# Kernel tuning notes

Hardware: AMD Instinct MI355X
Metric: run time of the kernel (lower is better)

The kernel has to match this reference:

```python
import jax, jax.numpy as jnp
import numpy as np
import math

NUM_BUCKETS = 32
MAX_DISTANCE = 128
N_HEADS = 16
D_KV = 64
ATTN_SCALE = True


def _relative_position_bucket(relative_position, num_buckets=NUM_BUCKETS, max_distance=MAX_DISTANCE):
    # bidirectional (encoder) variant
    nb = num_buckets // 2
    buckets = (relative_position > 0).astype(jnp.int32) * nb
    rp = jnp.abs(relative_position)
    max_exact = nb // 2
    is_small = rp < max_exact
    rp_large = max_exact + (
        jnp.log(rp.astype(jnp.float32) / max_exact)
        / math.log(max_distance / max_exact)
        * (nb - max_exact)
    ).astype(jnp.int32)
    rp_large = jnp.minimum(rp_large, nb - 1)
    buckets = buckets + jnp.where(is_small, rp, rp_large)
    return buckets


def compute_bias(rel_bias_emb, q_len, k_len):
    ctx = jnp.arange(q_len)[:, None]
    mem = jnp.arange(k_len)[None, :]
    bucket = _relative_position_bucket(mem - ctx)  # [q,k] int32 in [0,32)
    values = rel_bias_emb[bucket]                  # [q,k,H]
    return jnp.transpose(values, (2, 0, 1))[None]  # [1,H,q,k]


def setup_inputs() -> dict:
    key = jax.random.key(0)
    k1, k2, k3, k4 = jax.random.split(key, 4)
    B, S, D = 2, 2048, 1024
    return {
        "hidden_states": jax.random.normal(k1, (B, S, D), jnp.float32),
        "attention_mask": jnp.ones((B, 1, S, S), jnp.float32),
        "W_qkv": jax.random.normal(k2, (D, 3 * D), jnp.float32) * 0.02,
        "W_o": jax.random.normal(k3, (D, D), jnp.float32) * 0.02,
        "rel_bias_emb": jax.random.normal(k4, (NUM_BUCKETS, N_HEADS), jnp.float32) * 0.02,
    }


def reference(hidden_states, attention_mask, W_qkv, W_o, rel_bias_emb):
    B, S, D = hidden_states.shape
    # fused QKV projection (no bias), then split as in split_tensor_along_last_dim
    qkv = jnp.einsum("bsd,de->bse", hidden_states, W_qkv)
    q, k, v = jnp.split(qkv, 3, axis=-1)
    # [b,s,H*d] -> [b,H,s,d]
    def to_heads(t):
        return jnp.transpose(t.reshape(B, S, N_HEADS, D_KV), (0, 2, 1, 3))
    q, k, v = to_heads(q), to_heads(k), to_heads(v)
    scores = jnp.einsum("bhqd,bhkd->bhqk", q, k)
    if ATTN_SCALE:
        scores = scores / math.sqrt(D_KV)
    position_bias = compute_bias(rel_bias_emb, S, S)  # [1,H,S,S]
    scores = scores * attention_mask + (-10000.0 * (1.0 - attention_mask) + position_bias)
    probs = jax.nn.softmax(scores, axis=-1)  # dropout = eval mode (identity)
    ctx = jnp.einsum("bhqk,bhkd->bhqd", probs, v)
    ctx = jnp.transpose(ctx, (0, 2, 1, 3)).reshape(B, S, N_HEADS * D_KV)
    attn_output = jnp.einsum("bse,ed->bsd", ctx, W_o)
    return attn_output
```

## Files before the change

### kernel.cpp

```cpp
#include <hip/hip_runtime.h>
#include <cstdint>

#define DEV static __device__ __forceinline__

typedef __bf16 bf16x8 __attribute__((ext_vector_type(8)));
typedef __bf16 bf16x4 __attribute__((ext_vector_type(4)));
typedef short  s16x4  __attribute__((ext_vector_type(4)));
typedef float  f32x4  __attribute__((ext_vector_type(4)));

#define VM_WAIT4 asm volatile("s_waitcnt vmcnt(4)" ::: "memory")
#define VM_WAIT3 asm volatile("s_waitcnt vmcnt(3)" ::: "memory")
#define VM_WAIT0 asm volatile("s_waitcnt vmcnt(0)" ::: "memory")

DEV unsigned short f32_bf16(float f) {
  union { float f; unsigned u; } v; v.f = f;
  unsigned r = v.u + 0x7FFFu + ((v.u >> 16) & 1u);
  return (unsigned short)(r >> 16);
}

DEV void gload16(const void* g, void* lds) {
  __builtin_amdgcn_global_load_lds((__attribute__((address_space(1))) void*)g,
                                   (__attribute__((address_space(3))) void*)lds,
                                   16, 0, 0);
}

DEV float bcast_lane(float v, int srclane) {
  union { float f; int i; } u; u.f = v;
  u.i = __builtin_amdgcn_ds_bpermute(srclane << 2, u.i);
  return u.f;
}

DEV void transpose_body(const float* __restrict__ W, unsigned short* __restrict__ WT,
                        int K, int N, int k0, int n0, float (*t)[65]) {
  int tn = threadIdx.x & 63, tk = threadIdx.x >> 6;
#pragma unroll
  for (int i = 0; i < 64; i += 4)
    t[tk + i][tn] = W[(size_t)(k0 + tk + i) * N + n0 + tn];
  __syncthreads();
  int k2 = (threadIdx.x & 31) * 2, n = threadIdx.x >> 5;
#pragma unroll
  for (int i = 0; i < 64; i += 8) {
    int nn = n + i;
    unsigned o = (unsigned)f32_bf16(t[k2][nn]) | ((unsigned)f32_bf16(t[k2 + 1][nn]) << 16);
    *(unsigned*)&WT[(size_t)(n0 + nn) * K + k0 + k2] = o;
  }
}

__global__ void __launch_bounds__(256) prologue(const float* __restrict__ hs,
                                                unsigned short* __restrict__ hB,
                                                const float* __restrict__ wqkv,
                                                unsigned short* __restrict__ wqT,
                                                const float* __restrict__ wo,
                                                unsigned short* __restrict__ woT,
                                                const float* __restrict__ mask,
                                                int* __restrict__ flag) {
  __shared__ float t[64][65];
  const int bid = blockIdx.x;
  if (bid < 4096) {
    int i = bid * 256 + threadIdx.x;
    float4 v = ((const float4*)hs)[i];
    uint2 o;
    o.x = (unsigned)f32_bf16(v.x) | ((unsigned)f32_bf16(v.y) << 16);
    o.y = (unsigned)f32_bf16(v.z) | ((unsigned)f32_bf16(v.w) << 16);
    ((uint2*)hB)[i] = o;
  } else if (bid < 4864) {
    int tt = bid - 4096;
    transpose_body(wqkv, wqT, 1024, 3072, (tt & 15) * 64, (tt >> 4) * 64, t);
  } else if (bid < 5120) {
    int tt = bid - 4864;
    transpose_body(wo, woT, 1024, 1024, (tt & 15) * 64, (tt >> 4) * 64, t);
  } else {
    size_t i = ((size_t)(bid - 5120) * 256 + threadIdx.x) * 4;
    float4 v = *(const float4*)(mask + i);
    if (v.x != 1.0f || v.y != 1.0f || v.z != 1.0f || v.w != 1.0f) atomicOr(flag, 1);
  }
}

template <int MODE, int TN, bool TRANS>
DEV void gemm_body(const unsigned short* __restrict__ A,
                   const unsigned short* __restrict__ BT,
                   float* __restrict__ Cout,
                   unsigned short* __restrict__ Qb,
                   unsigned short* __restrict__ Kb,
                   unsigned short* __restrict__ VTb,
                   int bm, int bn, int M, int N, int K,
                   unsigned short* As, unsigned short* Bs) {
  constexpr int NT = TN / 32;
  constexpr int ASZ = 128 * 32, BSZ = TN * 32;
  const int tid = threadIdx.x, wave = tid >> 6, lane = tid & 63;
  const int l = lane & 15, quad = lane >> 4;
  const int wm = (wave & 1) * 64, wn = (wave >> 1) * (TN >> 1);

  const int srowA = wave * 32 + (lane >> 2);
  const int sswzA = ((lane & 3) ^ (srowA & 3)) * 8;
  const int srowB = (TN == 128) ? srowA : (wave * 16 + (lane >> 2));
  const int sswzB = ((lane & 3) ^ (srowB & 3)) * 8;
  const unsigned short* pA = A + (size_t)(bm * 128 + srowA) * K + sswzA;
  const unsigned short* pB = BT + (size_t)(bn * TN + srowB) * K + sswzB;
  const int ldsA0 = (wave * 32) * 32;
  const int ldsA1 = (wave * 32 + 16) * 32;
  const int ldsB0 = (TN == 128 ? wave * 32 : wave * 16) * 32;
  const int ldsB1 = (wave * 32 + 16) * 32;

  auto stage = [&](int buf) {
    gload16(pA, &As[buf * ASZ + ldsA0]);
    gload16(pA + (size_t)16 * K, &As[buf * ASZ + ldsA1]);
    gload16(pB, &Bs[buf * BSZ + ldsB0]);
    if (TN == 128) gload16(pB + (size_t)16 * K, &Bs[buf * BSZ + ldsB1]);
    pA += 32; pB += 32;
  };

  f32x4 acc[4][NT];
#pragma unroll
  for (int i = 0; i < 4; i++)
#pragma unroll
    for (int j = 0; j < NT; j++) { f32x4 z = {0.f, 0.f, 0.f, 0.f}; acc[i][j] = z; }

  stage(0);
  stage(1);

  const int nkt = K >> 5;
  for (int kt = 0; kt < nkt; kt++) {
    const int cur = kt % 3;
    if (kt != nkt - 1) {
      if (TN == 128) { VM_WAIT4; } else { VM_WAIT3; }
    } else {
      VM_WAIT0;
    }
    __builtin_amdgcn_s_barrier();
    __builtin_amdgcn_sched_barrier(0);
    if (kt + 2 < nkt) stage((kt + 2) % 3);
    bf16x8 af[4], bv[NT];
#pragma unroll
    for (int mt = 0; mt < 4; mt++) {
      int r = wm + mt * 16 + l;
      af[mt] = *(const bf16x8*)&As[cur * ASZ + r * 32 + ((quad ^ (r & 3)) * 8)];
    }
#pragma unroll
    for (int nt = 0; nt < NT; nt++) {
      int r = wn + nt * 16 + l;
      bv[nt] = *(const bf16x8*)&Bs[cur * BSZ + r * 32 + ((quad ^ (r & 3)) * 8)];
    }
#pragma unroll
    for (int mt = 0; mt < 4; mt++)
#pragma unroll
      for (int nt = 0; nt < NT; nt++) {
        if (TRANS)
          acc[mt][nt] = __builtin_amdgcn_mfma_f32_16x16x32_bf16(bv[nt], af[mt], acc[mt][nt], 0, 0, 0);
        else
          acc[mt][nt] = __builtin_amdgcn_mfma_f32_16x16x32_bf16(af[mt], bv[nt], acc[mt][nt], 0, 0, 0);
      }
  }

#pragma unroll
  for (int nt = 0; nt < NT; nt++) {
#pragma unroll
    for (int mt = 0; mt < 4; mt++) {
      if (TRANS) {
        const int s = bm * 128 + wm + mt * 16 + l;
        const int col = bn * TN + wn + nt * 16 + quad * 4;
        if (MODE == 0) {
          *(float4*)&Cout[(size_t)s * N + col] = *(float4*)&acc[mt][nt];
        } else {
          const int bb = s >> 11, sl = s & 2047;
          unsigned short* dst = (col < 1024) ? Qb : Kb;
          const int c = col & 1023;
          const size_t off = ((size_t)(bb * 16 + (c >> 6)) * 2048 + sl) * 64 + (c & 63);
          bf16x4 pk;
#pragma unroll
          for (int r = 0; r < 4; r++) pk[r] = (__bf16)acc[mt][nt][r];
          *(bf16x4*)&dst[off] = pk;
        }
      } else {
        const int col = bn * TN + wn + nt * 16 + l;
        const int row0 = bm * 128 + wm + mt * 16 + quad * 4;
        const int bb = row0 >> 11, s = row0 & 2047;
        const int c = col - 2048;
        const int sl = s & 127;
        const int snew = (s & ~127) | (sl & 0x63) | ((sl & 0x0C) << 1) | ((sl & 0x10) >> 2);
        const size_t off = ((size_t)(bb * 16 + (c >> 6)) * 64 + (c & 63)) * 2048 + snew;
        bf16x4 pk;
#pragma unroll
        for (int r = 0; r < 4; r++) pk[r] = (__bf16)acc[mt][nt][r];
        *(bf16x4*)&VTb[off] = pk;
      }
    }
  }
}

__global__ void __launch_bounds__(256) gemm_qkv(const unsigned short* __restrict__ A,
                                                const unsigned short* __restrict__ BT,
                                                unsigned short* __restrict__ Qb,
                                                unsigned short* __restrict__ Kb,
                                                unsigned short* __restrict__ VTb,
                                                int M, int N, int K) {
  __shared__ __align__(16) unsigned short As[3][128 * 32];
  __shared__ __align__(16) unsigned short Bs[3][128 * 32];
  const int bm = blockIdx.x, bn = blockIdx.y;
  if (bn < 16)
    gemm_body<2, 128, true>(A, BT, nullptr, Qb, Kb, VTb, bm, bn, M, N, K, &As[0][0], &Bs[0][0]);
  else
    gemm_body<2, 128, false>(A, BT, nullptr, Qb, Kb, VTb, bm, bn, M, N, K, &As[0][0], &Bs[0][0]);
}

__global__ void __launch_bounds__(256) gemm_out(const unsigned short* __restrict__ A,
                                                const unsigned short* __restrict__ BT,
                                                float* __restrict__ Cout,
                                                int M, int N, int K) {
  __shared__ __align__(16) unsigned short As[3][128 * 32];
  __shared__ __align__(16) unsigned short Bs[3][64 * 32];
  gemm_body<0, 64, true>(A, BT, Cout, nullptr, nullptr, nullptr,
                         blockIdx.x, blockIdx.y, M, N, K, &As[0][0], &Bs[0][0]);
}

__global__ void __launch_bounds__(512, 4) attn(const unsigned short* __restrict__ Qb,
                                               const unsigned short* __restrict__ Kb,
                                               const unsigned short* __restrict__ VTb,
                                               const float* __restrict__ mask,
                                               const float* __restrict__ emb,
                                               const int* __restrict__ mflag,
                                               unsigned short* __restrict__ ctx) {
  __shared__ __align__(16) unsigned short KV[2][16384];
  __shared__ float biasLUT[512];

  const float LOG2E = 1.4426950408889634f;
  const float c1 = 0.125f * LOG2E;
  const float C2 = 10000.0f * LOG2E;
  const int tid = threadIdx.x, wave = tid >> 6, lane = tid & 63;
  const int l = lane & 15, quad = lane >> 4;
  const int wq = wave & 3, wk = wave >> 2;
  const int bh = blockIdx.x & 31, qt = blockIdx.x >> 5;
  const int b = bh >> 4, h = bh & 15;
  const int q0 = qt * 128;

  {
    int i = tid;
    int rel = i - 256;
    int rp = rel < 0 ? -rel : rel;
    int off = rp < 8 ? rp
                     : 8 + (rp >= 12) + (rp >= 16) + (rp >= 23) + (rp >= 32) +
                           (rp >= 46) + (rp >= 64) + (rp >= 91);
    int bucket = (rel > 0 ? 16 : 0) + off;
    biasLUT[i] = emb[bucket * 16 + h] * LOG2E;
  }
  const float satL = emb[15 * 16 + h] * LOG2E;
  const float satH = emb[31 * 16 + h] * LOG2E;
  const int masked = *mflag;

  const unsigned short* qb  = Qb  + ((size_t)(b * 16 + h) * 2048 + q0) * 64;
  const unsigned short* kb  = Kb  + (size_t)(b * 16 + h) * 2048 * 64;
  const unsigned short* vtb = VTb + (size_t)(b * 16 + h) * 64 * 2048;
  const float* mbase = mask + (size_t)b * 2048 * 2048;

  const int rw8 = lane >> 3, c8s = lane & 7;
  const int rw16 = lane >> 4, c16 = lane & 15;

#pragma unroll
  for (int j = 0; j < 2; j++) {
    int row = wave * 16 + j * 8 + rw8;
    gload16(qb + (size_t)row * 64 + ((c8s ^ (row & 7)) * 8), &KV[1][(wave * 16 + j * 8) * 64]);
  }
#pragma unroll
  for (int j = 0; j < 2; j++) {
    int row = wave * 16 + j * 8 + rw8;
    gload16(kb + (size_t)row * 64 + ((c8s ^ (row & 7)) * 8), &KV[0][(wave * 16 + j * 8) * 64]);
  }
#pragma unroll
  for (int j = 0; j < 2; j++) {
    int drow = wave * 8 + j * 4 + rw16;
    gload16(vtb + (size_t)drow * 2048 + ((c16 ^ (drow & 7)) * 8),
            &KV[0][8192 + (wave * 8 + j * 4) * 128]);
  }
  __syncthreads();

  bf16x8 qf[2][2];
#pragma unroll
  for (int mtq = 0; mtq < 2; mtq++)
#pragma unroll
    for (int ks = 0; ks < 2; ks++) {
      int row = wq * 32 + mtq * 16 + l;
      qf[mtq][ks] = *(const bf16x8*)&KV[1][row * 64 + (((ks * 4 + quad) ^ (row & 7)) * 8)];
    }
  __syncthreads();

#pragma unroll
  for (int j = 0; j < 2; j++) {
    int row = wave * 16 + j * 8 + rw8;
    gload16(kb + (size_t)(128 + row) * 64 + ((c8s ^ (row & 7)) * 8),
            &KV[1][(wave * 16 + j * 8) * 64]);
  }
#pragma unroll
  for (int j = 0; j < 2; j++) {
    int drow = wave * 8 + j * 4 + rw16;
    gload16(vtb + (size_t)drow * 2048 + 128 + ((c16 ^ (drow & 7)) * 8),
            &KV[1][8192 + (wave * 8 + j * 4) * 128]);
  }

  float lr[2] = {0.f, 0.f};
  f32x4 Oa[2][4];
#pragma unroll
  for (int mtq = 0; mtq < 2; mtq++)
#pragma unroll
    for (int dt = 0; dt < 4; dt++) { f32x4 z = {0.f, 0.f, 0.f, 0.f}; Oa[mtq][dt] = z; }

  for (int kt = 0; kt < 16; kt++) {
    const int k0 = kt * 128;
    const unsigned short* Ks  = KV[kt & 1];
    const unsigned short* VTs = KV[kt & 1] + 8192;

    const int d0 = k0 - q0;
    const bool sat = (d0 >= 256) || (d0 <= -256);
    const float bias_u = d0 > 0 ? satH : satL;
    const int ibase = 256 + d0 + wk * 64 + quad * 4 - wq * 32 - l;

#pragma unroll
    for (int p = 0; p < 2; p++) {
      bf16x8 pa8[2];
#pragma unroll
      for (int t = 0; t < 2; t++) {
        const int ntk = p * 2 + t;
        int row = wk * 64 + ntk * 16 + l;
        bf16x8 kf0 = *(const bf16x8*)&Ks[row * 64 + ((quad ^ (row & 7)) * 8)];
        bf16x8 kf1 = *(const bf16x8*)&Ks[row * 64 + (((4 + quad) ^ (row & 7)) * 8)];
#pragma unroll
        for (int mtq = 0; mtq < 2; mtq++) {
          f32x4 s = {0.f, 0.f, 0.f, 0.f};
          __builtin_amdgcn_s_setprio(1);
          s = __builtin_amdgcn_mfma_f32_16x16x32_bf16(kf0, qf[mtq][0], s, 0, 0, 0);
          s = __builtin_amdgcn_mfma_f32_16x16x32_bf16(kf1, qf[mtq][1], s, 0, 0, 0);
          __builtin_amdgcn_s_setprio(0);

          const int ib = ibase + ntk * 16 - mtq * 16;
          if (!masked) {
            if (sat) {
#pragma unroll
              for (int r = 0; r < 4; r++) s[r] = fmaf(s[r], c1, bias_u);
            } else {
#pragma unroll
              for (int r = 0; r < 4; r++) s[r] = fmaf(s[r], c1, biasLUT[ib + r]);
            }
          } else {
            const int qg = q0 + wq * 32 + mtq * 16 + l;
            const int kg = k0 + wk * 64 + ntk * 16 + quad * 4;
            float4 mv4 = *(const float4*)&mbase[(size_t)qg * 2048 + kg];
#pragma unroll
            for (int r = 0; r < 4; r++) {
              float mv = r == 0 ? mv4.x : (r == 1 ? mv4.y : (r == 2 ? mv4.z : mv4.w));
              float bias = sat ? bias_u : biasLUT[ib + r];
              s[r] = fmaf(s[r], mv * c1, fmaf(mv, C2, bias - C2));
            }
          }
          float ls = 0.f;
#pragma unroll
          for (int r = 0; r < 4; r++) {
            float pv = __builtin_amdgcn_exp2f(s[r]);
            ls += pv;
            pa8[mtq][t * 4 + r] = (__bf16)pv;
          }
          lr[mtq] += ls;
        }
      }

      __builtin_amdgcn_s_setprio(1);
#pragma unroll
      for (int dt = 0; dt < 4; dt++) {
        int row = dt * 16 + l;
        bf16x8 w = *(const bf16x8*)&VTs[row * 128 + (((wk * 8 + p * 4 + quad) ^ (l & 7)) * 8)];
#pragma unroll
        for (int mtq = 0; mtq < 2; mtq++)
          Oa[mtq][dt] = __builtin_amdgcn_mfma_f32_16x16x32_bf16(pa8[mtq], w, Oa[mtq][dt], 0, 0, 0);
      }
      __builtin_amdgcn_s_setprio(0);
    }

    __syncthreads();
    if (kt + 2 < 16) {
      const int kn = (kt + 2) * 128;
      unsigned short* dst = (unsigned short*)KV[kt & 1];
#pragma unroll
      for (int j = 0; j < 2; j++) {
        int row = wave * 16 + j * 8 + rw8;
        gload16(kb + (size_t)(kn + row) * 64 + ((c8s ^ (row & 7)) * 8),
                &dst[(wave * 16 + j * 8) * 64]);
      }
#pragma unroll
      for (int j = 0; j < 2; j++) {
        int drow = wave * 8 + j * 4 + rw16;
        gload16(vtb + (size_t)drow * 2048 + kn + ((c16 ^ (drow & 7)) * 8),
                &dst[8192 + (wave * 8 + j * 4) * 128]);
      }
    }
  }

  float* Of = (float*)KV;
  float* Lf = Of + 8192;
  if (wk == 1) {
#pragma unroll
    for (int mtq = 0; mtq < 2; mtq++) {
      float v = lr[mtq];
      v += __shfl_xor(v, 16);
      v += __shfl_xor(v, 32);
      if (quad == 0) Lf[wq * 32 + mtq * 16 + l] = v;
#pragma unroll
      for (int dt = 0; dt < 4; dt++)
#pragma unroll
        for (int r = 0; r < 4; r++)
          Of[(wq * 32 + mtq * 16 + quad * 4 + r) * 64 + dt * 16 + l] = Oa[mtq][dt][r];
    }
  }
  __syncthreads();
  if (wk == 0) {
#pragma unroll
    for (int mtq = 0; mtq < 2; mtq++) {
      float v = lr[mtq];
      v += __shfl_xor(v, 16);
      v += __shfl_xor(v, 32);
      v += Lf[wq * 32 + mtq * 16 + l];
      const float inv = 1.0f / v;
#pragma unroll
      for (int r = 0; r < 4; r++) {
        float i_bc = bcast_lane(inv, quad * 4 + r);
        const int qg = q0 + wq * 32 + mtq * 16 + quad * 4 + r;
#pragma unroll
        for (int dt = 0; dt < 4; dt++) {
          float o = Oa[mtq][dt][r] +
                    Of[(wq * 32 + mtq * 16 + quad * 4 + r) * 64 + dt * 16 + l];
          ctx[(size_t)(b * 2048 + qg) * 1024 + h * 64 + dt * 16 + l] = f32_bf16(o * i_bc);
        }
      }
    }
  }
}

extern "C" void kernel_launch(void* const* d_in, const int* in_sizes, int n_in,
                              void* d_out, int out_size, void* d_ws, size_t ws_size,
                              hipStream_t stream) {
  const float* hs   = (const float*)d_in[0];
  const float* mask = (const float*)d_in[1];
  const float* wqkv = (const float*)d_in[2];
  const float* wo   = (const float*)d_in[3];
  const float* emb  = (const float*)d_in[4];
  float* out = (float*)d_out;

  char* ws = (char*)d_ws;
  unsigned short* hB  = (unsigned short*)(ws);
  unsigned short* ctx = (unsigned short*)(ws);
  unsigned short* wqT = (unsigned short*)(ws + 8388608);
  unsigned short* woT = (unsigned short*)(ws + 14680064);
  unsigned short* Qb  = (unsigned short*)(ws + 16777216);
  unsigned short* Kb  = (unsigned short*)(ws + 25165824);
  unsigned short* VTb = (unsigned short*)(ws + 33554432);
  int* mflag          = (int*)(ws + 41943040);
  if (ws_size < 41943044) return;

  hipMemsetAsync(mflag, 0, 4, stream);
  prologue<<<13312, 256, 0, stream>>>(hs, hB, wqkv, wqT, wo, woT, mask, mflag);
  gemm_qkv<<<dim3(32, 24), 256, 0, stream>>>(hB, wqT, Qb, Kb, VTb, 4096, 3072, 1024);
  attn<<<512, 512, 0, stream>>>(Qb, Kb, VTb, mask, emb, mflag, ctx);
  gemm_out<<<dim3(32, 16), 256, 0, stream>>>(ctx, woT, out, 4096, 1024, 1024);
}
```

Before: 201.1 us.

## Load V fragments directly from global memory and vectorize bias LUT reads

The V^T tile is no longer staged through shared memory. Each wave now reads its bf16x8 V fragments straight from global memory into registers inside the inner loop, which halves the KV shared buffer. The relative-position bias table is expanded into a 4-wide float4 LUT so each score fragment does one shared-memory read instead of four scalar reads. The smaller shared-memory footprint could allow more blocks per CU, but V loads now expose global latency inside the compute loop and are strided, with no prefetch.

```diff
diff --git a/kernel.cpp b/kernel.cpp
--- a/kernel.cpp
+++ b/kernel.cpp
@@ -220,8 +220,9 @@
                                                const float* __restrict__ emb,
                                                const int* __restrict__ mflag,
                                                unsigned short* __restrict__ ctx) {
-  __shared__ __align__(16) unsigned short KV[2][16384];
+  __shared__ __align__(16) unsigned short KV[2][8192];
   __shared__ float biasLUT[512];
+  __shared__ __align__(16) f32x4 biasLUT4[512];
 
   const float LOG2E = 1.4426950408889634f;
   const float c1 = 0.125f * LOG2E;
@@ -253,7 +254,6 @@
   const float* mbase = mask + (size_t)b * 2048 * 2048;
 
   const int rw8 = lane >> 3, c8s = lane & 7;
-  const int rw16 = lane >> 4, c16 = lane & 15;
 
 #pragma unroll
   for (int j = 0; j < 2; j++) {
@@ -265,13 +265,17 @@
     int row = wave * 16 + j * 8 + rw8;
     gload16(kb + (size_t)row * 64 + ((c8s ^ (row & 7)) * 8), &KV[0][(wave * 16 + j * 8) * 64]);
   }
-#pragma unroll
-  for (int j = 0; j < 2; j++) {
-    int drow = wave * 8 + j * 4 + rw16;
-    gload16(vtb + (size_t)drow * 2048 + ((c16 ^ (drow & 7)) * 8),
-            &KV[0][8192 + (wave * 8 + j * 4) * 128]);
-  }
   __syncthreads();
+
+  {
+    int i = tid;
+    f32x4 v4;
+    v4[0] = biasLUT[i];
+    v4[1] = biasLUT[i + 1 > 511 ? 511 : i + 1];
+    v4[2] = biasLUT[i + 2 > 511 ? 511 : i + 2];
+    v4[3] = biasLUT[i + 3 > 511 ? 511 : i + 3];
+    biasLUT4[i] = v4;
+  }
 
   bf16x8 qf[2][2];
 #pragma unroll
@@ -289,12 +293,6 @@
     gload16(kb + (size_t)(128 + row) * 64 + ((c8s ^ (row & 7)) * 8),
             &KV[1][(wave * 16 + j * 8) * 64]);
   }
-#pragma unroll
-  for (int j = 0; j < 2; j++) {
-    int drow = wave * 8 + j * 4 + rw16;
-    gload16(vtb + (size_t)drow * 2048 + 128 + ((c16 ^ (drow & 7)) * 8),
-            &KV[1][8192 + (wave * 8 + j * 4) * 128]);
-  }
 
   float lr[2] = {0.f, 0.f};
   f32x4 Oa[2][4];
@@ -305,8 +303,7 @@
 
   for (int kt = 0; kt < 16; kt++) {
     const int k0 = kt * 128;
-    const unsigned short* Ks  = KV[kt & 1];
-    const unsigned short* VTs = KV[kt & 1] + 8192;
+    const unsigned short* Ks = KV[kt & 1];
 
     const int d0 = k0 - q0;
     const bool sat = (d0 >= 256) || (d0 <= -256);
@@ -315,6 +312,12 @@
 
 #pragma unroll
     for (int p = 0; p < 2; p++) {
+      bf16x8 vw[4];
+#pragma unroll
+      for (int dt = 0; dt < 4; dt++)
+        vw[dt] = *(const bf16x8*)&vtb[(size_t)(dt * 16 + l) * 2048 + k0 +
+                                      (wk * 8 + p * 4 + quad) * 8];
+
       bf16x8 pa8[2];
 #pragma unroll
       for (int t = 0; t < 2; t++) {
@@ -331,13 +334,15 @@
           __builtin_amdgcn_s_setprio(0);
 
           const int ib = ibase + ntk * 16 - mtq * 16;
+          f32x4 bv4 = {0.f, 0.f, 0.f, 0.f};
+          if (!sat) bv4 = biasLUT4[ib];
           if (!masked) {
             if (sat) {
 #pragma unroll
               for (int r = 0; r < 4; r++) s[r] = fmaf(s[r], c1, bias_u);
             } else {
 #pragma unroll
-              for (int r = 0; r < 4; r++) s[r] = fmaf(s[r], c1, biasLUT[ib + r]);
+              for (int r = 0; r < 4; r++) s[r] = fmaf(s[r], c1, bv4[r]);
             }
           } else {
             const int qg = q0 + wq * 32 + mtq * 16 + l;
@@ -346,7 +351,7 @@
 #pragma unroll
             for (int r = 0; r < 4; r++) {
               float mv = r == 0 ? mv4.x : (r == 1 ? mv4.y : (r == 2 ? mv4.z : mv4.w));
-              float bias = sat ? bias_u : biasLUT[ib + r];
+              float bias = sat ? bias_u : bv4[r];
               s[r] = fmaf(s[r], mv * c1, fmaf(mv, C2, bias - C2));
             }
           }
@@ -363,13 +368,10 @@
 
       __builtin_amdgcn_s_setprio(1);
 #pragma unroll
-      for (int dt = 0; dt < 4; dt++) {
-        int row = dt * 16 + l;
-        bf16x8 w = *(const bf16x8*)&VTs[row * 128 + (((wk * 8 + p * 4 + quad) ^ (l & 7)) * 8)];
+      for (int dt = 0; dt < 4; dt++)
 #pragma unroll
         for (int mtq = 0; mtq < 2; mtq++)
-          Oa[mtq][dt] = __builtin_amdgcn_mfma_f32_16x16x32_bf16(pa8[mtq], w, Oa[mtq][dt], 0, 0, 0);
-      }
+          Oa[mtq][dt] = __builtin_amdgcn_mfma_f32_16x16x32_bf16(pa8[mtq], vw[dt], Oa[mtq][dt], 0, 0, 0);
       __builtin_amdgcn_s_setprio(0);
     }
 
@@ -383,17 +385,11 @@
         gload16(kb + (size_t)(kn + row) * 64 + ((c8s ^ (row & 7)) * 8),
                 &dst[(wave * 16 + j * 8) * 64]);
       }
-#pragma unroll
-      for (int j = 0; j < 2; j++) {
-        int drow = wave * 8 + j * 4 + rw16;
-        gload16(vtb + (size_t)drow * 2048 + kn + ((c16 ^ (drow & 7)) * 8),
-                &dst[8192 + (wave * 8 + j * 4) * 128]);
-      }
     }
   }
 
   float* Of = (float*)KV;
-  float* Lf = Of + 8192;
+  float* Lf = biasLUT;
   if (wk == 1) {
 #pragma unroll
     for (int mtq = 0; mtq < 2; mtq++) {
```

After: 275.6 us. 37.1% more time.
